# Optimization experiments

Hardware: AMD Instinct MI355X
Metric: run time of the kernel (lower is better)

The kernel has to match this reference:

```python
import jax, jax.numpy as jnp
import numpy as np

# Dims: B=8, C=64, H=W=256. 1x1 conv QKV projections (channel-mixing matmuls).

def setup_inputs() -> dict:
    key = jax.random.key(0)
    ks = jax.random.split(key, 7)
    B, C, H, W = 8, 64, 256, 256
    scale = 1.0 / np.sqrt(C)
    x = jax.random.normal(ks[0], (B, C, H, W), dtype=jnp.float32)
    wq = jax.random.normal(ks[1], (C, C), dtype=jnp.float32) * scale
    bq = jax.random.normal(ks[2], (C,), dtype=jnp.float32) * 0.01
    wk = jax.random.normal(ks[3], (C, C), dtype=jnp.float32) * scale
    bk = jax.random.normal(ks[4], (C,), dtype=jnp.float32) * 0.01
    wv = jax.random.normal(ks[5], (C, C), dtype=jnp.float32) * scale
    bv = jax.random.normal(ks[6], (C,), dtype=jnp.float32) * 0.01
    gamma = jnp.full((1,), 2.0, dtype=jnp.float32)  # nn.Parameter(FloatTensor([2]))
    return {"x": x, "wq": wq, "bq": bq, "wk": wk, "bk": bk, "wv": wv, "bv": bv, "gamma": gamma}


def reference(x, wq, bq, wk, bk, wv, bv, gamma):
    # 1x1 convs == per-pixel channel mixing
    Q = jnp.einsum('bchw,oc->bohw', x, wq) + bq[None, :, None, None]
    K = jnp.einsum('bchw,oc->bohw', x, wk) + bk[None, :, None, None]
    V = jnp.einsum('bchw,oc->bohw', x, wv) + bv[None, :, None, None]
    g = jax.nn.sigmoid(gamma)[0]  # sigmoid(2.0) > 0, eye-bias always applied
    # att[b,c,h,g] = sum_w Q[b,c,h,w] * K[b,c,g,w]  (key transposed on dims 2,3)
    att = jnp.einsum('bchw,bcgw->bchg', Q, K)
    H = att.shape[2]
    att = att + g * jnp.eye(H, dtype=att.dtype)
    # NOTE: softmax over the QUERY axis (dim=2), faithful to torch source
    att = jax.nn.softmax(att, axis=2)
    out = jnp.einsum('bchg,bcgw->bchw', att, V)
    return out
```

## Files before the change

### kernel.cpp

```cpp
#include <hip/hip_runtime.h>

typedef _Float16 f16x8 __attribute__((ext_vector_type(8)));
typedef _Float16 f16x4 __attribute__((ext_vector_type(4)));
typedef float    f32x4 __attribute__((ext_vector_type(4)));
typedef unsigned int u32x4 __attribute__((ext_vector_type(4)));

typedef const __attribute__((address_space(1))) void gvoid_t;
typedef __attribute__((address_space(3))) void lvoid_t;

__device__ __forceinline__ void lds_barrier() {
    asm volatile("s_waitcnt lgkmcnt(0)" ::: "memory");
    __builtin_amdgcn_sched_barrier(0);
    __builtin_amdgcn_s_barrier();
    __builtin_amdgcn_sched_barrier(0);
}

#define W_OFF   0
#define XA_OFF  24576
#define XB_OFF  40960
#define OUT_OFF 57344

__global__ __launch_bounds__(256, 2) void proj_qkv_mfma(
    const float* __restrict__ x,
    const float* __restrict__ wq, const float* __restrict__ bq,
    const float* __restrict__ wk, const float* __restrict__ bk,
    const float* __restrict__ wv, const float* __restrict__ bv,
    _Float16* __restrict__ Qh, _Float16* __restrict__ Kh, _Float16* __restrict__ Vh,
    const int rstride)
{
    __shared__ __align__(16) unsigned char lds[81920];

    const int tid  = threadIdx.x;
    const int lane = tid & 63;
    const int wid  = tid >> 6;
    const int q4   = lane >> 4;
    const int l15  = lane & 15;

    const int pg0  = blockIdx.x << 10;
    const int bb   = pg0 >> 16;
    const int pix0 = pg0 & 65535;
    const float* xb = x + ((size_t)bb << 22);

    const int sc = tid >> 5;
    const int sslot = tid & 31;

    float bld[12];
#pragma unroll
    for (int ot = 0; ot < 12; ++ot) {
        const int mat = ot >> 2;
        const float* bs = (mat == 0) ? bq : (mat == 1) ? bk : bv;
        bld[ot] = bs[((ot & 3) << 4) + l15];
    }

#pragma unroll
    for (int it = 0; it < 12; ++it) {
        const int idx  = (it << 8) + tid;
        const int orow = idx >> 4;
        const int s    = idx & 15;
        const int mat  = orow >> 6;
        const float* wsrc = (mat == 0) ? wq : (mat == 1) ? wk : wv;
        const f32x4 v = *(const f32x4*)(wsrc + ((orow & 63) << 6) + (s << 2));
        f16x4 h;
#pragma unroll
        for (int j = 0; j < 4; ++j) h[j] = (_Float16)v[j];
        const int a = ((orow << 7) + (s << 3)) ^ ((orow & 7) << 4);
        *(f16x4*)(lds + W_OFF + a) = h;
    }

    {
        f32x4 xv[8];
#pragma unroll
        for (int it = 0; it < 8; ++it) {
            const int c = (it << 3) + sc;
            xv[it] = *(const f32x4*)(xb + ((size_t)c << 16) + pix0 + (sslot << 2));
        }
#pragma unroll
        for (int it = 0; it < 8; ++it) {
            const int c = (it << 3) + sc;
            f16x4 h;
#pragma unroll
            for (int j = 0; j < 4; ++j) h[j] = (_Float16)xv[it][j];
            const int a = ((c << 8) + (sslot << 3)) ^ (((c >> 3) & 7) << 4);
            *(f16x4*)(lds + XA_OFF + a) = h;
        }
    }
    __syncthreads();

    const int wpx = wid << 5;

    for (int t = 0; t < 8; ++t) {
        const int bufo = (t & 1) ? XB_OFF : XA_OFF;
        const int nbufo = (t & 1) ? XA_OFF : XB_OFF;
        const int pixT = pix0 + (t << 7);

        f32x4 xv[8];
        if (t < 7) {
            const int pixN = pixT + 128;
#pragma unroll
            for (int it = 0; it < 8; ++it) {
                const int c = (it << 3) + sc;
                xv[it] = *(const f32x4*)(xb + ((size_t)c << 16) + pixN + (sslot << 2));
            }
        }

        f16x8 af[2][2];
#pragma unroll
        for (int pt = 0; pt < 2; ++pt)
#pragma unroll
            for (int kc = 0; kc < 2; ++kc) {
                const int px = wpx + (pt << 4) + l15;
                f16x8 a;
#pragma unroll
                for (int j = 0; j < 8; ++j) {
                    const int c  = (kc << 5) + (q4 << 3) + j;
                    const int ad = ((c << 8) + (px << 1)) ^ (((c >> 3) & 7) << 4);
                    a[j] = *(const _Float16*)(lds + bufo + ad);
                }
                af[pt][kc] = a;
            }

#pragma unroll
        for (int rd = 0; rd < 2; ++rd) {
            if (rd) lds_barrier();
#pragma unroll
            for (int ot6 = 0; ot6 < 6; ++ot6) {
                const int ot  = rd * 6 + ot6;
                const int row = (ot << 4) + l15;
                const int rsw = (row & 7) << 4;
                const f16x8 bf0 = *(const f16x8*)(lds + W_OFF + (((row << 7) + (q4 << 4)) ^ rsw));
                const f16x8 bf1 = *(const f16x8*)(lds + W_OFF + (((row << 7) + 64 + (q4 << 4)) ^ rsw));
                const int oo  = (ot6 << 4) + l15;
                const int osw = (oo & 7) << 4;
#pragma unroll
                for (int pt = 0; pt < 2; ++pt) {
                    f32x4 acc = { bld[ot], bld[ot], bld[ot], bld[ot] };
                    acc = __builtin_amdgcn_mfma_f32_16x16x32_f16(af[pt][0], bf0, acc, 0, 0, 0);
                    acc = __builtin_amdgcn_mfma_f32_16x16x32_f16(af[pt][1], bf1, acc, 0, 0, 0);
                    f16x4 h;
#pragma unroll
                    for (int r = 0; r < 4; ++r) h[r] = (_Float16)acc[r];
                    const int px = wpx + (pt << 4) + (q4 << 2);
                    *(f16x4*)(lds + OUT_OFF + (((oo << 8) + (px << 1)) ^ osw)) = h;
                }
            }
            lds_barrier();

#pragma unroll
            for (int it = 0; it < 6; ++it) {
                const int idx = (it << 8) + tid;
                const int oo  = idx >> 4;
                const int sl  = idx & 15;
                const u32x4 vst = *(const u32x4*)(lds + OUT_OFF +
                    (((oo << 8) + (sl << 4)) ^ ((oo & 7) << 4)));
                const int ot  = rd * 6 + (oo >> 4);
                const int mat = ot >> 2;
                _Float16* ob = (mat == 0) ? Qh : (mat == 1) ? Kh : Vh;
                const int orow = ((ot & 3) << 4) + (oo & 15);
                u32x4* dst = (u32x4*)(ob + (size_t)((bb << 6) + orow) * rstride + pixT + (sl << 3));
                __builtin_nontemporal_store(vst, dst);
            }
        }

        if (t < 7) {
#pragma unroll
            for (int it = 0; it < 8; ++it) {
                const int c = (it << 3) + sc;
                f16x4 h;
#pragma unroll
                for (int j = 0; j < 4; ++j) h[j] = (_Float16)xv[it][j];
                const int a = ((c << 8) + (sslot << 3)) ^ (((c >> 3) & 7) << 4);
                *(f16x4*)(lds + nbufo + a) = h;
            }
        }
        lds_barrier();
    }
}

#define P_OFF  0
#define RED_OFF 131072
#define VT_OFF 131072

__global__ __launch_bounds__(1024, 4) void attn_rowsm(
    const _Float16* __restrict__ Qh, const _Float16* __restrict__ Kh,
    const _Float16* __restrict__ Vh, const float* __restrict__ gamma,
    float* __restrict__ out, const int rstride)
{
    __shared__ __align__(16) unsigned char lds[163840];

    const int tid  = threadIdx.x;
    const int lane = tid & 63;
    const int wid  = tid >> 6;
    const int wr   = wid >> 2;
    const int wc   = wid & 3;
    const int q4   = lane >> 4;
    const int l15  = lane & 15;
    const size_t qbase = (size_t)blockIdx.x * rstride;

    const f32x4 fzero = {0.f, 0.f, 0.f, 0.f};
    f32x4 acc[4][4];
#pragma unroll
    for (int i = 0; i < 4; ++i)
#pragma unroll
        for (int j = 0; j < 4; ++j) acc[i][j] = fzero;

    auto dma_chunk = [&](int buf, int c) {
#pragma unroll
        for (int i = 0; i < 2; ++i) {
            const int idx = (((wid << 1) + i) << 10);
            const int h   = (idx >> 7) + (lane >> 3);
            const int sl  = lane & 7;
            const int kin = (sl << 3) ^ ((h & 7) << 3);
            const size_t src = qbase + (size_t)h * 256 + c * 64 + kin;
            __builtin_amdgcn_global_load_lds((gvoid_t*)(Qh + src),
                (lvoid_t*)(lds + buf + idx), 16, 0, 0);
            __builtin_amdgcn_global_load_lds((gvoid_t*)(Kh + src),
                (lvoid_t*)(lds + buf + 32768 + idx), 16, 0, 0);
        }
    };
    auto qk_chunk = [&](int buf) {
#pragma unroll
        for (int sub = 0; sub < 2; ++sub) {
            f16x8 bf[4];
#pragma unroll
            for (int ni = 0; ni < 4; ++ni) {
                const int g = (wc << 6) + (ni << 4) + l15;
                bf[ni] = *(const f16x8*)(lds + buf + 32768 + (g << 7) +
                         (((sub << 6) + (q4 << 4)) ^ ((g & 7) << 4)));
            }
#pragma unroll
            for (int mi = 0; mi < 4; ++mi) {
                const int h = (wr << 6) + (mi << 4) + l15;
                const f16x8 afr = *(const f16x8*)(lds + buf + (h << 7) +
                         (((sub << 6) + (q4 << 4)) ^ ((h & 7) << 4)));
#pragma unroll
                for (int ni = 0; ni < 4; ++ni)
                    acc[mi][ni] = __builtin_amdgcn_mfma_f32_16x16x32_f16(afr, bf[ni], acc[mi][ni], 0, 0, 0);
            }
        }
    };

    dma_chunk(0, 0);
    __builtin_amdgcn_sched_barrier(0);
#pragma unroll
    for (int c = 0; c < 4; ++c) {
        const int buf  = (c & 1) << 16;
        const int nbuf = ((c + 1) & 1) << 16;
        if (c < 3) dma_chunk(nbuf, c + 1);
        __builtin_amdgcn_sched_barrier(0);
        if (c < 3) { asm volatile("s_waitcnt vmcnt(4)" ::: "memory"); }
        else       { asm volatile("s_waitcnt vmcnt(0)" ::: "memory"); }
        __builtin_amdgcn_sched_barrier(0);
        lds_barrier();
        qk_chunk(buf);
        lds_barrier();
    }

    const int gp = tid >> 5;
    const int wo = tid & 31;
    uint4 vd0 = *(const uint4*)(Vh + qbase + (size_t)(gp << 1) * 256 + wo * 8);
    uint4 vd1 = *(const uint4*)(Vh + qbase + (size_t)((gp << 1) + 1) * 256 + wo * 8);

    const float g_sig = 1.0f / (1.0f + __expf(-gamma[0]));
    if (wr == wc) {
        const int rn = l15 - (q4 << 2);
        if (rn >= 0 && rn < 4) {
#pragma unroll
            for (int mi = 0; mi < 4; ++mi) acc[mi][mi][rn] += g_sig;
        }
    }

    float* red = (float*)(lds + RED_OFF);
    float cmx[4], cinv[4];

    lds_barrier();
#pragma unroll
    for (int ni = 0; ni < 4; ++ni) {
        float m = -3.0e38f;
#pragma unroll
        for (int mi = 0; mi < 4; ++mi)
#pragma unroll
            for (int r = 0; r < 4; ++r) m = fmaxf(m, acc[mi][ni][r]);
        m = fmaxf(m, __shfl_xor(m, 16));
        m = fmaxf(m, __shfl_xor(m, 32));
        cmx[ni] = m;
        if (q4 == 0) red[wr * 256 + (wc << 6) + (ni << 4) + l15] = m;
    }
    lds_barrier();
#pragma unroll
    for (int ni = 0; ni < 4; ++ni) {
        const int col = (wc << 6) + (ni << 4) + l15;
        float m = red[col];
        m = fmaxf(m, red[256 + col]);
        m = fmaxf(m, red[512 + col]);
        m = fmaxf(m, red[768 + col]);
        cmx[ni] = m;
    }
    lds_barrier();
#pragma unroll
    for (int ni = 0; ni < 4; ++ni) {
        float s = 0.f;
#pragma unroll
        for (int mi = 0; mi < 4; ++mi)
#pragma unroll
            for (int r = 0; r < 4; ++r) {
                const float e = __expf(acc[mi][ni][r] - cmx[ni]);
                acc[mi][ni][r] = e;
                s += e;
            }
        s += __shfl_xor(s, 16);
        s += __shfl_xor(s, 32);
        if (q4 == 0) red[wr * 256 + (wc << 6) + (ni << 4) + l15] = s;
    }
    lds_barrier();
#pragma unroll
    for (int ni = 0; ni < 4; ++ni) {
        const int col = (wc << 6) + (ni << 4) + l15;
        cinv[ni] = 1.0f / (red[col] + red[256 + col] + red[512 + col] + red[768 + col]);
    }

#pragma unroll
    for (int mi = 0; mi < 4; ++mi) {
        const int hbase = (wr << 6) + (mi << 4) + (q4 << 2);
#pragma unroll
        for (int r = 0; r < 4; ++r) {
            const int h  = hbase + r;
            const int hb = h << 9;
            const int sw = ((h & 3) << 4) ^ (((h >> 2) & 3) << 5);
#pragma unroll
            for (int ni = 0; ni < 4; ++ni) {
                const int g = (wc << 6) + (ni << 4) + l15;
                *(_Float16*)(lds + P_OFF + ((hb + (g << 1)) ^ sw)) =
                    (_Float16)(acc[mi][ni][r] * cinv[ni]);
            }
        }
    }

#pragma unroll
    for (int i = 0; i < 4; ++i)
#pragma unroll
        for (int j = 0; j < 4; ++j) acc[i][j] = fzero;

    auto v_scatter = [&](const uint4& a, const uint4& b) {
        const unsigned short* e0 = (const unsigned short*)&a;
        const unsigned short* e1 = (const unsigned short*)&b;
#pragma unroll
        for (int j = 0; j < 8; ++j) {
            const int w  = (wo << 3) + j;
            const int fw = ((w & 7) ^ ((w >> 3) & 7)) << 4;
            const unsigned int pk = (unsigned int)e0[j] | ((unsigned int)e1[j] << 16);
            *(unsigned int*)(lds + VT_OFF + (((w << 7) + (gp << 2)) ^ fw)) = pk;
        }
    };
    auto pv_chunk = [&](int gc) {
#pragma unroll
        for (int sub = 0; sub < 2; ++sub) {
            f16x8 bf[4];
#pragma unroll
            for (int ni = 0; ni < 4; ++ni) {
                const int w  = (wc << 6) + (ni << 4) + l15;
                const int fw = ((w & 7) ^ ((w >> 3) & 7)) << 4;
                bf[ni] = *(const f16x8*)(lds + VT_OFF + (w << 7) +
                         (((sub << 6) + (q4 << 4)) ^ fw));
            }
#pragma unroll
            for (int mi = 0; mi < 4; ++mi) {
                const int h  = (wr << 6) + (mi << 4) + l15;
                const int sw = ((h & 3) << 4) ^ (((h >> 2) & 3) << 5);
                const f16x8 afr = *(const f16x8*)(lds + P_OFF + (h << 9) +
                    ((((gc + (sub << 5) + (q4 << 3)) << 1)) ^ sw));
#pragma unroll
                for (int ni = 0; ni < 4; ++ni)
                    acc[mi][ni] = __builtin_amdgcn_mfma_f32_16x16x32_f16(afr, bf[ni], acc[mi][ni], 0, 0, 0);
            }
        }
    };

    for (int gc = 0; gc < 256; gc += 64) {
        lds_barrier();
        v_scatter(vd0, vd1);
        if (gc < 192) {
            const size_t vgn = qbase + (size_t)(gc + 64 + (gp << 1)) * 256 + wo * 8;
            vd0 = *(const uint4*)(Vh + vgn);
            vd1 = *(const uint4*)(Vh + vgn + 256);
        }
        lds_barrier();
        pv_chunk(gc);
    }

    float* op = out + ((size_t)blockIdx.x << 16);
#pragma unroll
    for (int pass = 0; pass < 2; ++pass) {
        lds_barrier();
#pragma unroll
        for (int mi2 = 0; mi2 < 2; ++mi2) {
            const int mi = pass * 2 + mi2;
#pragma unroll
            for (int r = 0; r < 4; ++r) {
                const int lr = (wr << 5) + (mi2 << 4) + (q4 << 2) + r;
                const int sw = (lr & 7) << 4;
#pragma unroll
                for (int ni = 0; ni < 4; ++ni) {
                    const int w = (wc << 6) + (ni << 4) + l15;
                    *(float*)(lds + P_OFF + (((lr << 10) + (w << 2)) ^ sw)) =
                        acc[mi][ni][r];
                }
            }
        }
        lds_barrier();
#pragma unroll
        for (int it = 0; it < 8; ++it) {
            const int idx = (it << 10) + tid;
            const int row = idx >> 6;
            const int sl  = idx & 63;
            const u32x4 v = *(const u32x4*)(lds + P_OFF +
                (((row << 10) + (sl << 4)) ^ ((row & 7) << 4)));
            const int h = ((row >> 5) << 6) + (pass << 5) + (row & 31);
            u32x4* dst = (u32x4*)(op + (h << 8) + (sl << 2));
            __builtin_nontemporal_store(v, dst);
        }
    }
}

extern "C" void kernel_launch(void* const* d_in, const int* in_sizes, int n_in,
                              void* d_out, int out_size, void* d_ws, size_t ws_size,
                              hipStream_t stream) {
    const float* x     = (const float*)d_in[0];
    const float* wq    = (const float*)d_in[1];
    const float* bq    = (const float*)d_in[2];
    const float* wk    = (const float*)d_in[3];
    const float* bk    = (const float*)d_in[4];
    const float* wv    = (const float*)d_in[5];
    const float* bv    = (const float*)d_in[6];
    const float* gamma = (const float*)d_in[7];
    float* out = (float*)d_out;

    int rstride = 65536 + 64;
    size_t perMat = (size_t)512 * rstride;
    if (perMat * 3 * sizeof(_Float16) > ws_size) {
        rstride = 65536;
        perMat = (size_t)512 * rstride;
    }
    _Float16* Qh = (_Float16*)d_ws;
    _Float16* Kh = Qh + perMat;
    _Float16* Vh = Kh + perMat;

    proj_qkv_mfma<<<512, 256, 0, stream>>>(x, wq, bq, wk, bk, wv, bv, Qh, Kh, Vh, rstride);
    attn_rowsm<<<512, 1024, 0, stream>>>(Qh, Kh, Vh, gamma, out, rstride);
}
```

Measured before the change: 146.1 us.

## Process two slices per persistent block and prefetch next Q/K during epilogue

The attention kernel now launches 256 blocks that each handle two (b,c) slices. The Q/K chunks for the second slice are prefetched into LDS buffers 0 and 1 while the first slice's output epilogue is still running, with adjusted vmcnt waits. The output staging moves to the VT region and is split into eight smaller passes so it does not overwrite the prefetched buffers. This aims to hide global load latency between slices and amortize block startup, at the cost of half as many blocks, which may lower parallelism on a large GPU, and more barriers in the epilogue.

```diff
diff --git a/kernel.cpp b/kernel.cpp
--- a/kernel.cpp
+++ b/kernel.cpp
@@ -194,229 +194,250 @@
     const int wc   = wid & 3;
     const int q4   = lane >> 4;
     const int l15  = lane & 15;
-    const size_t qbase = (size_t)blockIdx.x * rstride;
-
-    const f32x4 fzero = {0.f, 0.f, 0.f, 0.f};
-    f32x4 acc[4][4];
-#pragma unroll
-    for (int i = 0; i < 4; ++i)
-#pragma unroll
-        for (int j = 0; j < 4; ++j) acc[i][j] = fzero;
-
-    auto dma_chunk = [&](int buf, int c) {
+
+    auto dma_chunk = [&](size_t qb, int buf, int c) {
 #pragma unroll
         for (int i = 0; i < 2; ++i) {
             const int idx = (((wid << 1) + i) << 10);
             const int h   = (idx >> 7) + (lane >> 3);
             const int sl  = lane & 7;
             const int kin = (sl << 3) ^ ((h & 7) << 3);
-            const size_t src = qbase + (size_t)h * 256 + c * 64 + kin;
+            const size_t src = qb + (size_t)h * 256 + c * 64 + kin;
             __builtin_amdgcn_global_load_lds((gvoid_t*)(Qh + src),
                 (lvoid_t*)(lds + buf + idx), 16, 0, 0);
             __builtin_amdgcn_global_load_lds((gvoid_t*)(Kh + src),
                 (lvoid_t*)(lds + buf + 32768 + idx), 16, 0, 0);
         }
     };
-    auto qk_chunk = [&](int buf) {
-#pragma unroll
-        for (int sub = 0; sub < 2; ++sub) {
-            f16x8 bf[4];
-#pragma unroll
-            for (int ni = 0; ni < 4; ++ni) {
-                const int g = (wc << 6) + (ni << 4) + l15;
-                bf[ni] = *(const f16x8*)(lds + buf + 32768 + (g << 7) +
-                         (((sub << 6) + (q4 << 4)) ^ ((g & 7) << 4)));
-            }
-#pragma unroll
-            for (int mi = 0; mi < 4; ++mi) {
-                const int h = (wr << 6) + (mi << 4) + l15;
-                const f16x8 afr = *(const f16x8*)(lds + buf + (h << 7) +
-                         (((sub << 6) + (q4 << 4)) ^ ((h & 7) << 4)));
-#pragma unroll
-                for (int ni = 0; ni < 4; ++ni)
-                    acc[mi][ni] = __builtin_amdgcn_mfma_f32_16x16x32_f16(afr, bf[ni], acc[mi][ni], 0, 0, 0);
-            }
-        }
-    };
-
-    dma_chunk(0, 0);
+
+    const float g_sig = 1.0f / (1.0f + __expf(-gamma[0]));
+
+    dma_chunk((size_t)blockIdx.x * rstride, 0, 0);
+    dma_chunk((size_t)blockIdx.x * rstride, 65536, 1);
     __builtin_amdgcn_sched_barrier(0);
-#pragma unroll
-    for (int c = 0; c < 4; ++c) {
-        const int buf  = (c & 1) << 16;
-        const int nbuf = ((c + 1) & 1) << 16;
-        if (c < 3) dma_chunk(nbuf, c + 1);
-        __builtin_amdgcn_sched_barrier(0);
-        if (c < 3) { asm volatile("s_waitcnt vmcnt(4)" ::: "memory"); }
-        else       { asm volatile("s_waitcnt vmcnt(0)" ::: "memory"); }
-        __builtin_amdgcn_sched_barrier(0);
-        lds_barrier();
-        qk_chunk(buf);
-        lds_barrier();
-    }
-
-    const int gp = tid >> 5;
-    const int wo = tid & 31;
-    uint4 vd0 = *(const uint4*)(Vh + qbase + (size_t)(gp << 1) * 256 + wo * 8);
-    uint4 vd1 = *(const uint4*)(Vh + qbase + (size_t)((gp << 1) + 1) * 256 + wo * 8);
-
-    const float g_sig = 1.0f / (1.0f + __expf(-gamma[0]));
-    if (wr == wc) {
-        const int rn = l15 - (q4 << 2);
-        if (rn >= 0 && rn < 4) {
-#pragma unroll
-            for (int mi = 0; mi < 4; ++mi) acc[mi][mi][rn] += g_sig;
-        }
-    }
-
-    float* red = (float*)(lds + RED_OFF);
-    float cmx[4], cinv[4];
-
-    lds_barrier();
-#pragma unroll
-    for (int ni = 0; ni < 4; ++ni) {
-        float m = -3.0e38f;
-#pragma unroll
-        for (int mi = 0; mi < 4; ++mi)
-#pragma unroll
-            for (int r = 0; r < 4; ++r) m = fmaxf(m, acc[mi][ni][r]);
-        m = fmaxf(m, __shfl_xor(m, 16));
-        m = fmaxf(m, __shfl_xor(m, 32));
-        cmx[ni] = m;
-        if (q4 == 0) red[wr * 256 + (wc << 6) + (ni << 4) + l15] = m;
-    }
-    lds_barrier();
-#pragma unroll
-    for (int ni = 0; ni < 4; ++ni) {
-        const int col = (wc << 6) + (ni << 4) + l15;
-        float m = red[col];
-        m = fmaxf(m, red[256 + col]);
-        m = fmaxf(m, red[512 + col]);
-        m = fmaxf(m, red[768 + col]);
-        cmx[ni] = m;
-    }
-    lds_barrier();
-#pragma unroll
-    for (int ni = 0; ni < 4; ++ni) {
-        float s = 0.f;
-#pragma unroll
-        for (int mi = 0; mi < 4; ++mi)
+
+#pragma unroll
+    for (int it = 0; it < 2; ++it) {
+        const size_t qbase = (size_t)(blockIdx.x + (it << 8)) * rstride;
+
+        f32x4 acc[4][4];
+        const f32x4 fzero = {0.f, 0.f, 0.f, 0.f};
+#pragma unroll
+        for (int i = 0; i < 4; ++i)
+#pragma unroll
+            for (int j = 0; j < 4; ++j) acc[i][j] = fzero;
+
+        auto qk_chunk = [&](int buf) {
+#pragma unroll
+            for (int sub = 0; sub < 2; ++sub) {
+                f16x8 bf[4];
+#pragma unroll
+                for (int ni = 0; ni < 4; ++ni) {
+                    const int g = (wc << 6) + (ni << 4) + l15;
+                    bf[ni] = *(const f16x8*)(lds + buf + 32768 + (g << 7) +
+                             (((sub << 6) + (q4 << 4)) ^ ((g & 7) << 4)));
+                }
+#pragma unroll
+                for (int mi = 0; mi < 4; ++mi) {
+                    const int h = (wr << 6) + (mi << 4) + l15;
+                    const f16x8 afr = *(const f16x8*)(lds + buf + (h << 7) +
+                             (((sub << 6) + (q4 << 4)) ^ ((h & 7) << 4)));
+#pragma unroll
+                    for (int ni = 0; ni < 4; ++ni)
+                        acc[mi][ni] = __builtin_amdgcn_mfma_f32_16x16x32_f16(afr, bf[ni], acc[mi][ni], 0, 0, 0);
+                }
+            }
+        };
+
+#pragma unroll
+        for (int c = 0; c < 4; ++c) {
+            const int buf = (c & 1) << 16;
+            if (c == 1) dma_chunk(qbase, 0, 2);
+            if (c == 2) dma_chunk(qbase, 65536, 3);
+            __builtin_amdgcn_sched_barrier(0);
+            if (c == 0) { if (it == 0) asm volatile("s_waitcnt vmcnt(4)" ::: "memory");
+                          else         asm volatile("s_waitcnt vmcnt(20)" ::: "memory"); }
+            if (c == 1) { if (it == 0) asm volatile("s_waitcnt vmcnt(4)" ::: "memory");
+                          else         asm volatile("s_waitcnt vmcnt(20)" ::: "memory"); }
+            if (c == 2) asm volatile("s_waitcnt vmcnt(4)" ::: "memory");
+            if (c == 3) asm volatile("s_waitcnt vmcnt(0)" ::: "memory");
+            __builtin_amdgcn_sched_barrier(0);
+            lds_barrier();
+            qk_chunk(buf);
+            lds_barrier();
+        }
+
+        const int gp = tid >> 5;
+        const int wo = tid & 31;
+        uint4 vd0 = *(const uint4*)(Vh + qbase + (size_t)(gp << 1) * 256 + wo * 8);
+        uint4 vd1 = *(const uint4*)(Vh + qbase + (size_t)((gp << 1) + 1) * 256 + wo * 8);
+
+        if (wr == wc) {
+            const int rn = l15 - (q4 << 2);
+            if (rn >= 0 && rn < 4) {
+#pragma unroll
+                for (int mi = 0; mi < 4; ++mi) acc[mi][mi][rn] += g_sig;
+            }
+        }
+
+        float* red = (float*)(lds + RED_OFF);
+        float cmx[4], cinv[4];
+
+        lds_barrier();
+#pragma unroll
+        for (int ni = 0; ni < 4; ++ni) {
+            float m = -3.0e38f;
+#pragma unroll
+            for (int mi = 0; mi < 4; ++mi)
+#pragma unroll
+                for (int r = 0; r < 4; ++r) m = fmaxf(m, acc[mi][ni][r]);
+            m = fmaxf(m, __shfl_xor(m, 16));
+            m = fmaxf(m, __shfl_xor(m, 32));
+            cmx[ni] = m;
+            if (q4 == 0) red[wr * 256 + (wc << 6) + (ni << 4) + l15] = m;
+        }
+        lds_barrier();
+#pragma unroll
+        for (int ni = 0; ni < 4; ++ni) {
+            const int col = (wc << 6) + (ni << 4) + l15;
+            float m = red[col];
+            m = fmaxf(m, red[256 + col]);
+            m = fmaxf(m, red[512 + col]);
+            m = fmaxf(m, red[768 + col]);
+            cmx[ni] = m;
+        }
+        lds_barrier();
+#pragma unroll
+        for (int ni = 0; ni < 4; ++ni) {
+            float s = 0.f;
+#pragma unroll
+            for (int mi = 0; mi < 4; ++mi)
+#pragma unroll
+                for (int r = 0; r < 4; ++r) {
+                    const float e = __expf(acc[mi][ni][r] - cmx[ni]);
+                    acc[mi][ni][r] = e;
+                    s += e;
+                }
+            s += __shfl_xor(s, 16);
+            s += __shfl_xor(s, 32);
+            if (q4 == 0) red[wr * 256 + (wc << 6) + (ni << 4) + l15] = s;
+        }
+        lds_barrier();
+#pragma unroll
+        for (int ni = 0; ni < 4; ++ni) {
+            const int col = (wc << 6) + (ni << 4) + l15;
+            cinv[ni] = 1.0f / (red[col] + red[256 + col] + red[512 + col] + red[768 + col]);
+        }
+
+#pragma unroll
+        for (int mi = 0; mi < 4; ++mi) {
+            const int hbase = (wr << 6) + (mi << 4) + (q4 << 2);
 #pragma unroll
             for (int r = 0; r < 4; ++r) {
-                const float e = __expf(acc[mi][ni][r] - cmx[ni]);
-                acc[mi][ni][r] = e;
-                s += e;
-            }
-        s += __shfl_xor(s, 16);
-        s += __shfl_xor(s, 32);
-        if (q4 == 0) red[wr * 256 + (wc << 6) + (ni << 4) + l15] = s;
-    }
-    lds_barrier();
-#pragma unroll
-    for (int ni = 0; ni < 4; ++ni) {
-        const int col = (wc << 6) + (ni << 4) + l15;
-        cinv[ni] = 1.0f / (red[col] + red[256 + col] + red[512 + col] + red[768 + col]);
-    }
-
-#pragma unroll
-    for (int mi = 0; mi < 4; ++mi) {
-        const int hbase = (wr << 6) + (mi << 4) + (q4 << 2);
-#pragma unroll
-        for (int r = 0; r < 4; ++r) {
-            const int h  = hbase + r;
-            const int hb = h << 9;
-            const int sw = ((h & 3) << 4) ^ (((h >> 2) & 3) << 5);
-#pragma unroll
-            for (int ni = 0; ni < 4; ++ni) {
-                const int g = (wc << 6) + (ni << 4) + l15;
-                *(_Float16*)(lds + P_OFF + ((hb + (g << 1)) ^ sw)) =
-                    (_Float16)(acc[mi][ni][r] * cinv[ni]);
-            }
-        }
-    }
-
-#pragma unroll
-    for (int i = 0; i < 4; ++i)
-#pragma unroll
-        for (int j = 0; j < 4; ++j) acc[i][j] = fzero;
-
-    auto v_scatter = [&](const uint4& a, const uint4& b) {
-        const unsigned short* e0 = (const unsigned short*)&a;
-        const unsigned short* e1 = (const unsigned short*)&b;
-#pragma unroll
-        for (int j = 0; j < 8; ++j) {
-            const int w  = (wo << 3) + j;
-            const int fw = ((w & 7) ^ ((w >> 3) & 7)) << 4;
-            const unsigned int pk = (unsigned int)e0[j] | ((unsigned int)e1[j] << 16);
-            *(unsigned int*)(lds + VT_OFF + (((w << 7) + (gp << 2)) ^ fw)) = pk;
-        }
-    };
-    auto pv_chunk = [&](int gc) {
-#pragma unroll
-        for (int sub = 0; sub < 2; ++sub) {
-            f16x8 bf[4];
-#pragma unroll
-            for (int ni = 0; ni < 4; ++ni) {
-                const int w  = (wc << 6) + (ni << 4) + l15;
+                const int h  = hbase + r;
+                const int hb = h << 9;
+                const int sw = ((h & 3) << 4) ^ (((h >> 2) & 3) << 5);
+#pragma unroll
+                for (int ni = 0; ni < 4; ++ni) {
+                    const int g = (wc << 6) + (ni << 4) + l15;
+                    *(_Float16*)(lds + P_OFF + ((hb + (g << 1)) ^ sw)) =
+                        (_Float16)(acc[mi][ni][r] * cinv[ni]);
+                }
+            }
+        }
+
+#pragma unroll
+        for (int i = 0; i < 4; ++i)
+#pragma unroll
+            for (int j = 0; j < 4; ++j) acc[i][j] = fzero;
+
+        auto v_scatter = [&](const uint4& a, const uint4& b) {
+            const unsigned short* e0 = (const unsigned short*)&a;
+            const unsigned short* e1 = (const unsigned short*)&b;
+#pragma unroll
+            for (int j = 0; j < 8; ++j) {
+                const int w  = (wo << 3) + j;
                 const int fw = ((w & 7) ^ ((w >> 3) & 7)) << 4;
-                bf[ni] = *(const f16x8*)(lds + VT_OFF + (w << 7) +
-                         (((sub << 6) + (q4 << 4)) ^ fw));
-            }
-#pragma unroll
-            for (int mi = 0; mi < 4; ++mi) {
-                const int h  = (wr << 6) + (mi << 4) + l15;
-                const int sw = ((h & 3) << 4) ^ (((h >> 2) & 3) << 5);
-                const f16x8 afr = *(const f16x8*)(lds + P_OFF + (h << 9) +
-                    ((((gc + (sub << 5) + (q4 << 3)) << 1)) ^ sw));
-#pragma unroll
-                for (int ni = 0; ni < 4; ++ni)
-                    acc[mi][ni] = __builtin_amdgcn_mfma_f32_16x16x32_f16(afr, bf[ni], acc[mi][ni], 0, 0, 0);
-            }
-        }
-    };
-
-    for (int gc = 0; gc < 256; gc += 64) {
-        lds_barrier();
-        v_scatter(vd0, vd1);
-        if (gc < 192) {
-            const size_t vgn = qbase + (size_t)(gc + 64 + (gp << 1)) * 256 + wo * 8;
-            vd0 = *(const uint4*)(Vh + vgn);
-            vd1 = *(const uint4*)(Vh + vgn + 256);
-        }
-        lds_barrier();
-        pv_chunk(gc);
-    }
-
-    float* op = out + ((size_t)blockIdx.x << 16);
-#pragma unroll
-    for (int pass = 0; pass < 2; ++pass) {
-        lds_barrier();
-#pragma unroll
-        for (int mi2 = 0; mi2 < 2; ++mi2) {
-            const int mi = pass * 2 + mi2;
-#pragma unroll
-            for (int r = 0; r < 4; ++r) {
-                const int lr = (wr << 5) + (mi2 << 4) + (q4 << 2) + r;
-                const int sw = (lr & 7) << 4;
+                const unsigned int pk = (unsigned int)e0[j] | ((unsigned int)e1[j] << 16);
+                *(unsigned int*)(lds + VT_OFF + (((w << 7) + (gp << 2)) ^ fw)) = pk;
+            }
+        };
+        auto pv_chunk = [&](int gc) {
+#pragma unroll
+            for (int sub = 0; sub < 2; ++sub) {
+                f16x8 bf[4];
 #pragma unroll
                 for (int ni = 0; ni < 4; ++ni) {
-                    const int w = (wc << 6) + (ni << 4) + l15;
-                    *(float*)(lds + P_OFF + (((lr << 10) + (w << 2)) ^ sw)) =
-                        acc[mi][ni][r];
-                }
-            }
-        }
-        lds_barrier();
-#pragma unroll
-        for (int it = 0; it < 8; ++it) {
-            const int idx = (it << 10) + tid;
-            const int row = idx >> 6;
-            const int sl  = idx & 63;
-            const u32x4 v = *(const u32x4*)(lds + P_OFF +
-                (((row << 10) + (sl << 4)) ^ ((row & 7) << 4)));
-            const int h = ((row >> 5) << 6) + (pass << 5) + (row & 31);
-            u32x4* dst = (u32x4*)(op + (h << 8) + (sl << 2));
-            __builtin_nontemporal_store(v, dst);
+                    const int w  = (wc << 6) + (ni << 4) + l15;
+                    const int fw = ((w & 7) ^ ((w >> 3) & 7)) << 4;
+                    bf[ni] = *(const f16x8*)(lds + VT_OFF + (w << 7) +
+                             (((sub << 6) + (q4 << 4)) ^ fw));
+                }
+#pragma unroll
+                for (int mi = 0; mi < 4; ++mi) {
+                    const int h  = (wr << 6) + (mi << 4) + l15;
+                    const int sw = ((h & 3) << 4) ^ (((h >> 2) & 3) << 5);
+                    const f16x8 afr = *(const f16x8*)(lds + P_OFF + (h << 9) +
+                        ((((gc + (sub << 5) + (q4 << 3)) << 1)) ^ sw));
+#pragma unroll
+                    for (int ni = 0; ni < 4; ++ni)
+                        acc[mi][ni] = __builtin_amdgcn_mfma_f32_16x16x32_f16(afr, bf[ni], acc[mi][ni], 0, 0, 0);
+                }
+            }
+        };
+
+        for (int gc = 0; gc < 256; gc += 64) {
+            lds_barrier();
+            v_scatter(vd0, vd1);
+            if (gc < 192) {
+                const size_t vgn = qbase + (size_t)(gc + 64 + (gp << 1)) * 256 + wo * 8;
+                vd0 = *(const uint4*)(Vh + vgn);
+                vd1 = *(const uint4*)(Vh + vgn + 256);
+            }
+            lds_barrier();
+            pv_chunk(gc);
+        }
+
+        lds_barrier();
+        if (it == 0) {
+            const size_t qb2 = (size_t)(blockIdx.x + 256) * rstride;
+            dma_chunk(qb2, 0, 0);
+            dma_chunk(qb2, 65536, 1);
+            __builtin_amdgcn_sched_barrier(0);
+        }
+
+        float* op = out + ((size_t)(blockIdx.x + (it << 8)) << 16);
+#pragma unroll
+        for (int pass = 0; pass < 8; ++pass) {
+            lds_barrier();
+            if (wr == (pass >> 1)) {
+#pragma unroll
+                for (int mi2 = 0; mi2 < 2; ++mi2) {
+                    const int mi = ((pass & 1) << 1) + mi2;
+#pragma unroll
+                    for (int r = 0; r < 4; ++r) {
+                        const int lr = (mi2 << 4) + (q4 << 2) + r;
+                        const int sw = (lr & 7) << 4;
+#pragma unroll
+                        for (int ni = 0; ni < 4; ++ni) {
+                            const int w = (wc << 6) + (ni << 4) + l15;
+                            *(float*)(lds + VT_OFF + (((lr << 10) + (w << 2)) ^ sw)) =
+                                acc[mi][ni][r];
+                        }
+                    }
+                }
+            }
+            lds_barrier();
+#pragma unroll
+            for (int it2 = 0; it2 < 2; ++it2) {
+                const int idx = (it2 << 10) + tid;
+                const int row = idx >> 6;
+                const int sl  = idx & 63;
+                const u32x4 v = *(const u32x4*)(lds + VT_OFF +
+                    (((row << 10) + (sl << 4)) ^ ((row & 7) << 4)));
+                const int h = (pass << 5) + row;
+                __builtin_nontemporal_store(v, (u32x4*)(op + (h << 8) + (sl << 2)));
+            }
         }
     }
 }
@@ -445,5 +466,5 @@
     _Float16* Vh = Kh + perMat;
 
     proj_qkv_mfma<<<512, 256, 0, stream>>>(x, wq, bq, wk, bk, wv, bv, Qh, Kh, Vh, rstride);
-    attn_rowsm<<<512, 1024, 0, stream>>>(Qh, Kh, Vh, gamma, out, rstride);
+    attn_rowsm<<<256, 1024, 0, stream>>>(Qh, Kh, Vh, gamma, out, rstride);
 }
```

New measurement: 277.1 us. 89.8% more time.
